# Optimization experiments

Measured on AMD Instinct MI355X. Metric: run time of the kernel, lower is better.

## Reference

```python
import jax, jax.numpy as jnp
import numpy as np

B, L, D, H = 2, 2048, 2048, 16
HD = D // H          # head_dim = 128
LAT = HD // 4        # latent_dim = 32


def setup_inputs() -> dict:
    key = jax.random.key(0)
    ks = jax.random.split(key, 16)
    def w(k, shape, fan_in):
        return jax.random.normal(k, shape, jnp.float32) / np.float32(np.sqrt(fan_in))
    x = jax.random.normal(ks[0], (B, L, D), jnp.float32)
    # RoPE frequencies, stored as (cos, sin) pairs: [L, HD//2, 2]
    inv_freq = 1.0 / (10000.0 ** (np.arange(0, HD, 2, dtype=np.float32) / HD))
    ang = np.outer(np.arange(L, dtype=np.float32), inv_freq)
    freqs_cis = jnp.stack([jnp.asarray(np.cos(ang)), jnp.asarray(np.sin(ang))], axis=-1)
    return dict(
        x=x, freqs_cis=freqs_cis,
        Wq=w(ks[1], (D, D), D), bq=jnp.zeros((D,), jnp.float32),
        Wk=w(ks[2], (D, D), D), bk=jnp.zeros((D,), jnp.float32),
        Wv=w(ks[3], (D, D), D), bv=jnp.zeros((D,), jnp.float32),
        Wqc=w(ks[4], (LAT, HD), HD), bqc=jnp.zeros((LAT,), jnp.float32),
        Wkc=w(ks[5], (LAT, HD), HD), bkc=jnp.zeros((LAT,), jnp.float32),
        Wvc=w(ks[6], (LAT, HD), HD), bvc=jnp.zeros((LAT,), jnp.float32),
        Wd=w(ks[7], (HD, LAT), LAT), bd=jnp.zeros((HD,), jnp.float32),
        Wo=w(ks[8], (D, D), D), bo=jnp.zeros((D,), jnp.float32),
    )


def _rope(t, freqs_cis):
    # t: [B,H,L,HD]; freqs_cis: [L, HD//2, 2] (cos, sin)
    tp = t.reshape(t.shape[:-1] + (HD // 2, 2))
    a, b = tp[..., 0], tp[..., 1]
    cr = freqs_cis[:, :, 0]  # [L, HD//2]
    ci = freqs_cis[:, :, 1]
    ra = a * cr - b * ci
    rb = a * ci + b * cr
    return jnp.stack([ra, rb], axis=-1).reshape(t.shape)


def reference(x, freqs_cis, Wq, bq, Wk, bk, Wv, bv, Wqc, bqc, Wkc, bkc, Wvc, bvc, Wd, bd, Wo, bo):
    Bx, Lx, Dx = x.shape
    # QKV projections -> [B,H,L,HD]
    def proj(W, bias):
        return (x @ W.T + bias).reshape(Bx, Lx, H, HD).transpose(0, 2, 1, 3)
    q = proj(Wq, bq)
    k = proj(Wk, bk)
    v = proj(Wv, bv)
    q = _rope(q, freqs_cis)
    k = _rope(k, freqs_cis)
    # per-head compression to latent dim: [B,H,L,LAT]
    qc = q @ Wqc.T + bqc
    kc = k @ Wkc.T + bkc
    vc = v @ Wvc.T + bvc
    scores = jnp.einsum('bhie,bhje->bhij', qc, kc) / np.float32(np.sqrt(LAT))
    mask = jnp.triu(jnp.ones((Lx, Lx), bool), 1)  # future positions
    scores = jnp.where(mask, jnp.float32(-jnp.inf), scores)
    probs = jax.nn.softmax(scores, axis=-1)
    attn = jnp.einsum('bhij,bhje->bhie', probs, vc)  # [B,H,L,LAT]
    attn = attn @ Wd.T + bd                          # decompress -> [B,H,L,HD]
    attn = attn.transpose(0, 2, 1, 3).reshape(Bx, Lx, Dx)
    return attn @ Wo.T + bo
```

## Files before the change

kernel.cpp:

```cpp
#include <hip/hip_runtime.h>

typedef __attribute__((ext_vector_type(8))) __bf16 bf16x8;
typedef __attribute__((ext_vector_type(4))) __bf16 bf16x4;
typedef __attribute__((ext_vector_type(4))) float f32x4;
typedef __attribute__((ext_vector_type(16))) float f32x16;

#define LL 2048
#define DD 2048
#define HH 16
#define HDIM 128

__global__ __launch_bounds__(256)
void cvt_all(const float* __restrict__ x, const float* __restrict__ Wq,
             const float* __restrict__ Wk, const float* __restrict__ Wqc,
             const float* __restrict__ Wkc,
             __bf16* __restrict__ xb, __bf16* __restrict__ Wqb, __bf16* __restrict__ Wkb,
             __bf16* __restrict__ Wqcb, __bf16* __restrict__ Wkcb)
{
    size_t i = (size_t)blockIdx.x * 256 + threadIdx.x;
    const float* s; __bf16* d; size_t off;
    if (i < 2097152)      { s = x;   d = xb;   off = i; }
    else if (i < 3145728) { s = Wq;  d = Wqb;  off = i - 2097152; }
    else if (i < 4194304) { s = Wk;  d = Wkb;  off = i - 3145728; }
    else if (i < 4195328) { s = Wqc; d = Wqcb; off = i - 4194304; }
    else                  { s = Wkc; d = Wkcb; off = i - 4195328; }
    float4 v = *(const float4*)(s + off * 4);
    bf16x4 o = { (__bf16)v.x, (__bf16)v.y, (__bf16)v.z, (__bf16)v.w };
    *(bf16x4*)(d + off * 4) = o;
}

__global__ __launch_bounds__(256)
void build_wv_eff(const float* __restrict__ Wv, const float* __restrict__ Wvc,
                  const float* __restrict__ bv, const float* __restrict__ bvc,
                  __bf16* __restrict__ Wveff, float* __restrict__ bveff)
{
    __shared__ float WvcT[128][32];
    const int h = blockIdx.x, dc = blockIdx.y, tid = threadIdx.x;
    for (int i = tid; i < 4096; i += 256) WvcT[i & 127][i >> 7] = Wvc[i];
    __syncthreads();
    const int d  = dc * 64 + (tid & 63);
    const int o0 = (tid >> 6) * 8;
    float acc[8] = {};
    for (int j = 0; j < 128; ++j) {
        const float w = Wv[(size_t)(h * 128 + j) * 2048 + d];
        #pragma unroll
        for (int o = 0; o < 8; ++o) acc[o] += WvcT[j][o0 + o] * w;
    }
    #pragma unroll
    for (int o = 0; o < 8; ++o)
        Wveff[(size_t)(h * 32 + o0 + o) * 2048 + d] = (__bf16)acc[o];
    if (dc == 0 && tid < 32) {
        float s = bvc[tid];
        for (int j = 0; j < 128; ++j) s += WvcT[j][tid] * bv[h * 128 + j];
        bveff[h * 32 + tid] = s;
    }
}

__global__ __launch_bounds__(256)
void build_wo_eff(const float* __restrict__ Wo, const float* __restrict__ Wd,
                  __bf16* __restrict__ Woeff)
{
    __shared__ float WdL[128][32];
    const int dc = blockIdx.x, h = blockIdx.y, tid = threadIdx.x;
    for (int i = tid; i < 4096; i += 256) WdL[i >> 5][i & 31] = Wd[i];
    __syncthreads();
    const int dout = dc * 64 + (tid & 63);
    const int o0   = (tid >> 6) * 8;
    float acc[8] = {};
    const float* wrow = Wo + (size_t)dout * 2048 + h * 128;
    for (int u = 0; u < 128; ++u) {
        const float w = wrow[u];
        #pragma unroll
        for (int o = 0; o < 8; ++o) acc[o] += WdL[u][o0 + o] * w;
    }
    #pragma unroll
    for (int o = 0; o < 8; ++o)
        Woeff[(size_t)dout * 512 + h * 32 + o0 + o] = (__bf16)acc[o];
}

__global__ __launch_bounds__(256)
void build_bo_eff(const float* __restrict__ Wo, const float* __restrict__ bd,
                  const float* __restrict__ bo, float* __restrict__ boeff)
{
    __shared__ float bdL[128];
    const int tid = threadIdx.x;
    if (tid < 128) bdL[tid] = bd[tid];
    __syncthreads();
    const int d  = blockIdx.x * 32 + (tid >> 3);
    const int s0 = (tid & 7) * 64;
    float s = 0.f;
    const float* wrow = Wo + (size_t)d * 2048 + s0 * 4;
    for (int c4 = 0; c4 < 64; ++c4) {
        float4 wv = *(const float4*)(wrow + c4 * 4);
        const int cb = ((s0 + c4) * 4) & 127;
        s += wv.x * bdL[cb] + wv.y * bdL[cb + 1] + wv.z * bdL[cb + 2] + wv.w * bdL[cb + 3];
    }
    #pragma unroll
    for (int off = 4; off; off >>= 1) s += __shfl_down(s, off, 8);
    if ((tid & 7) == 0) boeff[d] = bo[d] + s;
}

typedef unsigned int u32;
typedef const __attribute__((address_space(1))) u32* gp_t;
typedef __attribute__((address_space(3))) u32* lp_t;
__device__ __forceinline__ void gload16(const __bf16* g, __bf16* l)
{
    __builtin_amdgcn_global_load_lds((gp_t)(const void*)g, (lp_t)(void*)l, 16, 0, 0);
}

#define MF16(a, b, c) __builtin_amdgcn_mfma_f32_16x16x32_bf16(a, b, c, 0, 0, 0)

__global__ __launch_bounds__(512, 2)
void gemm_qkv8(const __bf16* __restrict__ A,
               const __bf16* __restrict__ Wq, const __bf16* __restrict__ Wk,
               const __bf16* __restrict__ Wveff,
               const float* __restrict__ bq, const float* __restrict__ bk,
               const float* __restrict__ bveff,
               __bf16* __restrict__ qb, __bf16* __restrict__ kb, __bf16* __restrict__ vt)
{
    __shared__ __bf16 lds[4][2][8192];

    const int bid = blockIdx.x;
    const int xcd = bid & 7;
    const int jj  = bid >> 3;
    const int by  = xcd * 2 + (jj / 18);
    const int bx  = jj % 18;
    const int m0  = by * 256;
    const int which = (bx >= 16) ? 2 : (bx >> 3);
    const int nseg  = (which == 2) ? (bx - 16) * 256 : (bx & 7) * 256;
    const __bf16* W = which == 0 ? Wq : which == 1 ? Wk : Wveff;

    const int tid  = threadIdx.x;
    const int wid  = tid >> 6;
    const int lane = tid & 63;
    const int wr   = wid >> 2;
    const int wc   = wid & 3;
    const int l15  = lane & 15;
    const int l4   = lane >> 4;
    const int swz  = (l4 ^ (l15 & 3)) * 8;

    const int srl  = lane >> 2;
    const int scol = ((lane & 3) ^ (srl & 3)) * 8;
    const __bf16* gA0 = A + (size_t)(m0 + wid * 32 + srl) * 2048 + scol;
    const __bf16* gA1 = gA0 + (size_t)16 * 2048;
    const __bf16* gB0 = W + (size_t)(nseg + wid * 32 + srl) * 2048 + scol;
    const __bf16* gB1 = gB0 + (size_t)16 * 2048;

    #define STAGE_A(bb, kkv)                                           \
    {   __bf16* d_ = &lds[bb][0][(wid * 2) * 512];                     \
        gload16(gA0 + (kkv), d_);                                      \
        gload16(gA1 + (kkv), d_ + 512);                                \
    }
    #define STAGE_B(bb, kkv)                                           \
    {   __bf16* d_ = &lds[bb][1][(wid * 2) * 512];                     \
        gload16(gB0 + (kkv), d_);                                      \
        gload16(gB1 + (kkv), d_ + 512);                                \
    }
    #define RD_A(bb, mf) (*(const bf16x8*)&lds[bb][0][(wr * 128 + (mf) * 16 + l15) * 32 + swz])
    #define RD_B(bb, nf) (*(const bf16x8*)&lds[bb][1][(wc * 64 + (nf) * 16 + l15) * 32 + swz])

    f32x4 acc[8][4] = {};

    STAGE_A(0, 0)  STAGE_B(0, 0)
    STAGE_A(1, 32) STAGE_B(1, 32)
    STAGE_A(2, 64) STAGE_B(2, 64)

    #define TILE_BODY(bb, VMS, DOSTAGE, kkv)                                  \
    {                                                                         \
        const int b_ = (bb);                                                  \
        asm volatile("s_waitcnt vmcnt(" VMS ")" ::: "memory");                \
        __builtin_amdgcn_s_barrier();                                         \
        bf16x8 fa[8], fb[4];                                                  \
        _Pragma("unroll")                                                     \
        for (int mf = 0; mf < 8; ++mf) fa[mf] = RD_A(b_, mf);                 \
        fb[0] = RD_B(b_, 0); fb[1] = RD_B(b_, 1);                             \
        if (DOSTAGE) STAGE_A(((b_ + 3) & 3), (kkv))                           \
        asm volatile("s_waitcnt lgkmcnt(0)" ::: "memory");                    \
        __builtin_amdgcn_sched_barrier(0);                                    \
        __builtin_amdgcn_s_setprio(1);                                        \
        _Pragma("unroll")                                                     \
        for (int mf = 0; mf < 8; ++mf) {                                      \
            acc[mf][0] = MF16(fa[mf], fb[0], acc[mf][0]);                     \
            acc[mf][1] = MF16(fa[mf], fb[1], acc[mf][1]);                     \
        }                                                                     \
        __builtin_amdgcn_s_setprio(0);                                        \
        fb[2] = RD_B(b_, 2); fb[3] = RD_B(b_, 3);                             \
        if (DOSTAGE) STAGE_B(((b_ + 3) & 3), (kkv))                           \
        asm volatile("s_waitcnt lgkmcnt(0)" ::: "memory");                    \
        __builtin_amdgcn_sched_barrier(0);                                    \
        __builtin_amdgcn_s_setprio(1);                                        \
        _Pragma("unroll")                                                     \
        for (int mf = 0; mf < 8; ++mf) {                                      \
            acc[mf][2] = MF16(fa[mf], fb[2], acc[mf][2]);                     \
            acc[mf][3] = MF16(fa[mf], fb[3], acc[mf][3]);                     \
        }                                                                     \
        __builtin_amdgcn_s_setprio(0);                                        \
    }

    for (int t = 0; t < 61; ++t)
        TILE_BODY((t & 3), "8", true, (t + 3) * 32)
    TILE_BODY(1, "8", false, 0)
    TILE_BODY(2, "4", false, 0)
    TILE_BODY(3, "0", false, 0)

    #undef TILE_BODY
    #undef STAGE_A
    #undef STAGE_B
    #undef RD_A
    #undef RD_B

    if (which < 2) {
        __bf16* C = which ? kb : qb;
        const float* bb = which ? bk : bq;
        #pragma unroll
        for (int nf = 0; nf < 4; ++nf) {
            const int col = nseg + wc * 64 + nf * 16 + l15;
            const float bv = bb[col];
            #pragma unroll
            for (int mf = 0; mf < 8; ++mf) {
                const int row0 = m0 + wr * 128 + mf * 16 + l4 * 4;
                #pragma unroll
                for (int rr = 0; rr < 4; ++rr)
                    C[(size_t)(row0 + rr) * 2048 + col] = (__bf16)(acc[mf][nf][rr] + bv);
            }
        }
    } else {
        #pragma unroll
        for (int nf = 0; nf < 4; ++nf) {
            const int ncol = nseg + wc * 64 + nf * 16 + l15;
            const float bv = bveff[ncol];
            const int hh = ncol >> 5, oo = ncol & 31;
            #pragma unroll
            for (int mf = 0; mf < 8; ++mf) {
                const int row0 = m0 + wr * 128 + mf * 16 + l4 * 4;
                const int b = row0 >> 11, l0 = row0 & 2047;
                bf16x4 pk = { (__bf16)(acc[mf][nf][0] + bv), (__bf16)(acc[mf][nf][1] + bv),
                              (__bf16)(acc[mf][nf][2] + bv), (__bf16)(acc[mf][nf][3] + bv) };
                *(bf16x4*)(vt + ((size_t)((b * 16 + hh) * 32 + oo)) * 2048 + l0) = pk;
            }
        }
    }
}

__global__ __launch_bounds__(256)
void gemm_ao(const __bf16* __restrict__ ao, const __bf16* __restrict__ Woeff,
             const float* __restrict__ boeff, float* __restrict__ out)
{
    __shared__ __bf16 As[128][64];
    __shared__ __bf16 Bs[128][64];
    const int bid = blockIdx.x;
    const int x   = bid & 7;
    const int jj  = bid >> 3;
    const int bx  = x * 2 + (jj & 1);
    const int by  = jj >> 1;
    const int m0  = by * 128;
    const int n0  = bx * 128;

    const int tid  = threadIdx.x;
    const int wave = tid >> 6;
    const int lane = tid & 63;
    const int wr   = (wave >> 1) * 64;
    const int wc   = (wave & 1) * 64;
    const int lr   = lane & 15;
    const int lk   = (lane >> 4) * 8;
    const int srow = wave * 32 + (lane >> 3);
    const int scol = (lane & 7) * 8;

    f32x4 acc[4][4] = {};
    __bf16* lA = &As[wave * 32][0];
    __bf16* lB = &Bs[wave * 32][0];
    const __bf16* Ww = Woeff + (size_t)(n0 + srow) * 512 + scol;

    for (int k0 = 0; k0 < 512; k0 += 64) {
        const int kk = k0 + scol;
        const int hblk = kk >> 5, oo = kk & 31;
        #pragma unroll
        for (int j = 0; j < 4; ++j) {
            const int r = m0 + srow + j * 8;
            const int b = r >> 11, l = r & 2047;
            gload16(ao + ((size_t)((b << 4) + hblk) * 2048 + l) * 32 + oo, lA + j * 512);
            gload16(Ww + (size_t)(j * 8) * 512 + k0, lB + j * 512);
        }
        __syncthreads();
        #pragma unroll
        for (int ks = 0; ks < 2; ++ks) {
            bf16x8 af[4], bfr[4];
            #pragma unroll
            for (int m = 0; m < 4; ++m)
                af[m] = *(const bf16x8*)(&As[wr + m * 16 + lr][ks * 32 + lk]);
            #pragma unroll
            for (int n = 0; n < 4; ++n)
                bfr[n] = *(const bf16x8*)(&Bs[wc + n * 16 + lr][ks * 32 + lk]);
            #pragma unroll
            for (int m = 0; m < 4; ++m)
                #pragma unroll
                for (int n = 0; n < 4; ++n)
                    acc[m][n] = MF16(af[m], bfr[n], acc[m][n]);
        }
        __syncthreads();
    }

    const int orow = (lane >> 4) * 4;
    #pragma unroll
    for (int n = 0; n < 4; ++n) {
        const int col = n0 + wc + n * 16 + lr;
        const float bv = boeff[col];
        #pragma unroll
        for (int m = 0; m < 4; ++m) {
            #pragma unroll
            for (int r = 0; r < 4; ++r) {
                const int row = m0 + wr + m * 16 + orow + r;
                out[(size_t)row * 2048 + col] = acc[m][n][r] + bv;
            }
        }
    }
}

__global__ __launch_bounds__(256)
void latproj_mfma(const __bf16* __restrict__ qb, const __bf16* __restrict__ kb,
                  const __bf16* __restrict__ Wqcb, const __bf16* __restrict__ Wkcb,
                  const float* __restrict__ bq, const float* __restrict__ bk,
                  const float* __restrict__ fc,
                  __bf16* __restrict__ qc, __bf16* __restrict__ kc)
{
    const int which = blockIdx.y;
    const __bf16* in = which == 0 ? qb : kb;
    const __bf16* Wb = which == 0 ? Wqcb : Wkcb;
    const float*  bs = which == 0 ? bq : bk;

    const int wave = threadIdx.x >> 6;
    const int lane = threadIdx.x & 63;
    const int o    = lane & 31;
    const int hi   = lane >> 5;
    const int g0   = (blockIdx.x * 4 + wave) * 32;

    bf16x8 wf[8];
    #pragma unroll
    for (int ks = 0; ks < 8; ++ks)
        wf[ks] = *(const bf16x8*)(Wb + o * 128 + ks * 16 + hi * 8);

    const int g = g0 + o;
    const int b = g >> 15, h = (g >> 11) & 15, l = g & (LL - 1);
    const __bf16* arow = in + ((size_t)(b * LL + l)) * DD + h * HDIM;
    const float* fcr = fc + (size_t)l * 128;

    f32x16 C = {};
    #pragma unroll
    for (int ks = 0; ks < 8; ++ks) {
        bf16x8 af = *(const bf16x8*)(arow + ks * 16 + hi * 8);
        const float4 cA = *(const float4*)(fcr + (ks * 8 + hi * 4) * 2);
        const float4 cB = *(const float4*)(fcr + (ks * 8 + hi * 4) * 2 + 4);
        float a, bb_;
        a = (float)af[0]; bb_ = (float)af[1];
        af[0] = (__bf16)(a * cA.x - bb_ * cA.y); af[1] = (__bf16)(a * cA.y + bb_ * cA.x);
        a = (float)af[2]; bb_ = (float)af[3];
        af[2] = (__bf16)(a * cA.z - bb_ * cA.w); af[3] = (__bf16)(a * cA.w + bb_ * cA.z);
        a = (float)af[4]; bb_ = (float)af[5];
        af[4] = (__bf16)(a * cB.x - bb_ * cB.y); af[5] = (__bf16)(a * cB.y + bb_ * cB.x);
        a = (float)af[6]; bb_ = (float)af[7];
        af[6] = (__bf16)(a * cB.z - bb_ * cB.w); af[7] = (__bf16)(a * cB.w + bb_ * cB.z);
        C = __builtin_amdgcn_mfma_f32_32x32x16_bf16(af, wf[ks], C, 0, 0, 0);
    }

    const float bias = bs[o];
    const float QSCALE = 0.17677669529663689f * 1.44269504088896340f;
    __bf16* outp = (which == 0 ? qc : kc);
    #pragma unroll
    for (int r = 0; r < 16; ++r) {
        const int ro = (r & 3) + 8 * (r >> 2) + 4 * hi;
        float v = C[r] + bias;
        if (which == 0) v *= QSCALE;
        outp[(size_t)(g0 + ro) * 32 + o] = (__bf16)v;
    }
}

__device__ __forceinline__ unsigned pkbf2(float a, float b)
{
    union { __bf16 h[2]; unsigned u; } x;
    x.h[0] = (__bf16)a; x.h[1] = (__bf16)b;
    return x.u;
}

#if __has_builtin(__builtin_amdgcn_permlane32_swap)
typedef unsigned int uint2v __attribute__((ext_vector_type(2)));
__device__ __forceinline__ void plswap(unsigned a, unsigned b, unsigned& w_lo, unsigned& w_hi, int)
{
    uint2v r = __builtin_amdgcn_permlane32_swap(a, b, false, false);
    w_lo = r[0]; w_hi = r[1];
}
#else
__device__ __forceinline__ void plswap(unsigned a, unsigned b, unsigned& w_lo, unsigned& w_hi, int hi)
{
    unsigned ax = (unsigned)__shfl_xor((int)a, 32);
    unsigned bx = (unsigned)__shfl_xor((int)b, 32);
    w_lo = hi ? bx : a;
    w_hi = hi ? b  : ax;
}
#endif

__global__ __launch_bounds__(64)
void attn_part(const __bf16* __restrict__ qc, const __bf16* __restrict__ kc,
               const __bf16* __restrict__ vt,
               float* __restrict__ pm, float* __restrict__ pl, float* __restrict__ po)
{
    const int id  = blockIdx.x;
    const int bhl = id & 7;
    const int c   = id >> 3;
    const int bhh = c / 160;
    const int lin = c - bhh * 160;
    int s, ci;
    if (lin < 16)      { s = lin; ci = 0; }
    else if (lin < 48) { int q = lin - 16; s = 16 + (q >> 1); ci = q & 1; }
    else if (lin < 96) { int q = lin - 48; int d = q / 3; s = 32 + d; ci = q - d * 3; }
    else               { int q = lin - 96; s = 48 + (q >> 2); ci = q & 3; }
    const int bh = bhh * 8 + bhl;

    const int lane = threadIdx.x;
    const int qcol = lane & 31;
    const int hi   = lane >> 5;

    const __bf16* qbase = qc + ((size_t)bh * LL + (size_t)s * 32) * 32;
    const __bf16* kbase = kc + (size_t)bh * LL * 32;
    const __bf16* vbase = vt + (size_t)bh * 32 * LL;

    const bf16x8 qf0 = *(const bf16x8*)(qbase + qcol * 32 + hi * 8);
    const bf16x8 qf1 = *(const bf16x8*)(qbase + qcol * 32 + 16 + hi * 8);

    float m = -1e30f, lsum = 0.f;
    f32x16 O = {};

    const int t0 = ci * 16;
    const int t1 = min(s, t0 + 15);

    const __bf16* krow = kbase + (size_t)(t0 * 32 + qcol) * 32 + hi * 8;
    const __bf16* vrow = vbase + (size_t)qcol * LL + t0 * 32 + hi * 8;
    bf16x8 kc0 = *(const bf16x8*)(krow);
    bf16x8 kc1 = *(const bf16x8*)(krow + 16);
    bf16x8 vc0 = *(const bf16x8*)(vrow);
    bf16x8 vc1 = *(const bf16x8*)(vrow + 16);

    for (int t = t0; t <= t1; ++t) {
        const int tn = (t < t1) ? t + 1 : t;
        const __bf16* krn = kbase + (size_t)(tn * 32 + qcol) * 32 + hi * 8;
        const __bf16* vrn = vbase + (size_t)qcol * LL + tn * 32 + hi * 8;
        bf16x8 kn0 = *(const bf16x8*)(krn);
        bf16x8 kn1 = *(const bf16x8*)(krn + 16);
        bf16x8 vn0 = *(const bf16x8*)(vrn);
        bf16x8 vn1 = *(const bf16x8*)(vrn + 16);

        f32x16 S = {};
        S = __builtin_amdgcn_mfma_f32_32x32x16_bf16(kc0, qf0, S, 0, 0, 0);
        S = __builtin_amdgcn_mfma_f32_32x32x16_bf16(kc1, qf1, S, 0, 0, 0);

        if (t == s) {
            #pragma unroll
            for (int r = 0; r < 16; ++r) {
                const int kl = (r & 3) + 8 * (r >> 2) + 4 * hi;
                if (kl > qcol) S[r] = -1e30f;
            }
        }
        float tm = S[0];
        #pragma unroll
        for (int r = 1; r < 16; ++r) tm = fmaxf(tm, S[r]);
        tm = fmaxf(tm, __shfl_xor(tm, 32));
        const float mn = fmaxf(m, tm);
        const float fr = exp2f(m - mn);
        m = mn;
        float p[16]; float ls = 0.f;
        #pragma unroll
        for (int r = 0; r < 16; ++r) { p[r] = exp2f(S[r] - m); ls += p[r]; }
        lsum = lsum * fr + ls;
        #pragma unroll
        for (int r = 0; r < 16; ++r) O[r] *= fr;

        unsigned w[8];
        #pragma unroll
        for (int i = 0; i < 8; ++i) w[i] = pkbf2(p[2 * i], p[2 * i + 1]);
        union PF { unsigned u[4]; bf16x8 v; } pf1, pf2;
        plswap(w[0], w[2], pf1.u[0], pf1.u[2], hi);
        plswap(w[1], w[3], pf1.u[1], pf1.u[3], hi);
        plswap(w[4], w[6], pf2.u[0], pf2.u[2], hi);
        plswap(w[5], w[7], pf2.u[1], pf2.u[3], hi);

        O = __builtin_amdgcn_mfma_f32_32x32x16_bf16(vc0, pf1.v, O, 0, 0, 0);
        O = __builtin_amdgcn_mfma_f32_32x32x16_bf16(vc1, pf2.v, O, 0, 0, 0);

        kc0 = kn0; kc1 = kn1; vc0 = vn0; vc1 = vn1;
    }

    const float L = lsum + __shfl_xor(lsum, 32);
    const size_t g = (size_t)bh * LL + (size_t)s * 32 + qcol;
    const size_t slot = g * 4 + ci;
    if (hi == 0) { pm[slot] = m; pl[slot] = L; }
    float* pp = po + slot * 32;
    #pragma unroll
    for (int g4 = 0; g4 < 4; ++g4) {
        float4 v = { O[g4 * 4 + 0], O[g4 * 4 + 1], O[g4 * 4 + 2], O[g4 * 4 + 3] };
        *(float4*)(pp + g4 * 8 + 4 * hi) = v;
    }
}

__global__ __launch_bounds__(256)
void attn_comb(const float* __restrict__ pm, const float* __restrict__ pl,
               const float* __restrict__ po, __bf16* __restrict__ ao)
{
    const int g = blockIdx.x * 256 + threadIdx.x;
    const int i = g & (LL - 1);
    const int nch = (i >> 9) + 1;
    float m = -1e30f;
    for (int c = 0; c < nch; ++c) m = fmaxf(m, pm[(size_t)g * 4 + c]);
    float L = 0.f;
    float o[32] = {};
    for (int c = 0; c < nch; ++c) {
        const float w = exp2f(pm[(size_t)g * 4 + c] - m);
        L += w * pl[(size_t)g * 4 + c];
        const float* pp = po + ((size_t)g * 4 + c) * 32;
        #pragma unroll
        for (int d4 = 0; d4 < 8; ++d4) {
            float4 v = *(const float4*)(pp + d4 * 4);
            o[d4*4+0] += w * v.x; o[d4*4+1] += w * v.y;
            o[d4*4+2] += w * v.z; o[d4*4+3] += w * v.w;
        }
    }
    const float inv = 1.f / L;
    #pragma unroll
    for (int d8 = 0; d8 < 4; ++d8) {
        bf16x8 v;
        #pragma unroll
        for (int j = 0; j < 8; ++j) v[j] = (__bf16)(o[d8 * 8 + j] * inv);
        *(bf16x8*)(ao + (size_t)g * 32 + d8 * 8) = v;
    }
}

extern "C" void kernel_launch(void* const* d_in, const int* in_sizes, int n_in,
                              void* d_out, int out_size, void* d_ws, size_t ws_size,
                              hipStream_t stream)
{
    const float* x   = (const float*)d_in[0];
    const float* fc  = (const float*)d_in[1];
    const float* Wq  = (const float*)d_in[2];
    const float* bq  = (const float*)d_in[3];
    const float* Wk  = (const float*)d_in[4];
    const float* bk  = (const float*)d_in[5];
    const float* Wv  = (const float*)d_in[6];
    const float* bv  = (const float*)d_in[7];
    const float* Wqc = (const float*)d_in[8];
    const float* bqc = (const float*)d_in[9];
    const float* Wkc = (const float*)d_in[10];
    const float* bkc = (const float*)d_in[11];
    const float* Wvc = (const float*)d_in[12];
    const float* bvc = (const float*)d_in[13];
    const float* Wd  = (const float*)d_in[14];
    const float* bd  = (const float*)d_in[15];
    const float* Wo  = (const float*)d_in[16];
    const float* bo  = (const float*)d_in[17];
    float* out = (float*)d_out;

    const size_t MB = 1048576;
    char* w = (char*)d_ws;
    __bf16* xb    = (__bf16*)(w);
    __bf16* Wqb   = (__bf16*)(w + 16 * MB);
    __bf16* Wkb   = (__bf16*)(w + 24 * MB);
    __bf16* Wveff = (__bf16*)(w + 32 * MB);
    __bf16* qb    = (__bf16*)(w + 34 * MB);
    __bf16* kb    = (__bf16*)(w + 50 * MB);
    __bf16* qcbf  = (__bf16*)(w + 66 * MB);
    __bf16* kcbf  = (__bf16*)(w + 70 * MB);
    __bf16* vtbf  = (__bf16*)(w + 74 * MB);
    __bf16* aobf  = (__bf16*)(w + 78 * MB);
    __bf16* Wqcb  = (__bf16*)(w + 82 * MB);
    __bf16* Wkcb  = (__bf16*)(w + 82 * MB + 8192);
    __bf16* Woeff = (__bf16*)(w + 83 * MB);
    float*  boeff = (float*)(w + 85 * MB);
    float*  bveff = (float*)(w + 85 * MB + 8192);

    float* po = (float*)d_ws;
    float* pm = (float*)(w + 32 * MB);
    float* pl = (float*)(w + 33 * MB);

    if (ws_size < (size_t)90 * MB) return;

    cvt_all<<<16392, 256, 0, stream>>>(x, Wq, Wk, Wqc, Wkc, xb, Wqb, Wkb, Wqcb, Wkcb);
    build_wv_eff<<<dim3(16, 32), 256, 0, stream>>>(Wv, Wvc, bv, bvc, Wveff, bveff);
    build_wo_eff<<<dim3(32, 16), 256, 0, stream>>>(Wo, Wd, Woeff);
    build_bo_eff<<<64, 256, 0, stream>>>(Wo, bd, bo, boeff);

    gemm_qkv8<<<288, 512, 0, stream>>>(xb, Wqb, Wkb, Wveff, bq, bk, bveff, qb, kb, vtbf);

    latproj_mfma<<<dim3(512, 2), 256, 0, stream>>>(qb, kb, Wqcb, Wkcb, bqc, bkc, fc,
                                                   qcbf, kcbf);

    attn_part<<<5120, 64, 0, stream>>>(qcbf, kcbf, vtbf, pm, pl, po);
    attn_comb<<<256, 256, 0, stream>>>(pm, pl, po, aobf);

    gemm_ao<<<512, 256, 0, stream>>>(aobf, Woeff, boeff, out);
}
```

Measured before the change: 258.2 us.

## Shrink QKV GEMM tiles to 128x128 with 3-stage pipeline and more blocks

Replaces the 256x256-tile, 512-thread, 4-buffer QKV GEMM with a 128x128-tile, 256-thread kernel using a 3-buffer LDS ring and one barrier per K-step, launched as 1152 blocks instead of 288. The intent is better load balance across CUs, since 288 blocks underfill a 256-CU part in two waves, and higher occupancy (3 blocks per CU). The trade-off is lower arithmetic intensity per tile and more global and L2 traffic for A and W.

```diff
diff --git a/kernel.cpp b/kernel.cpp
--- a/kernel.cpp
+++ b/kernel.cpp
@@ -110,31 +110,32 @@
 
 #define MF16(a, b, c) __builtin_amdgcn_mfma_f32_16x16x32_bf16(a, b, c, 0, 0, 0)
 
-__global__ __launch_bounds__(512, 2)
-void gemm_qkv8(const __bf16* __restrict__ A,
-               const __bf16* __restrict__ Wq, const __bf16* __restrict__ Wk,
-               const __bf16* __restrict__ Wveff,
-               const float* __restrict__ bq, const float* __restrict__ bk,
-               const float* __restrict__ bveff,
-               __bf16* __restrict__ qb, __bf16* __restrict__ kb, __bf16* __restrict__ vt)
-{
-    __shared__ __bf16 lds[4][2][8192];
+__global__ __launch_bounds__(256, 3)
+void gemm_qkv(const __bf16* __restrict__ A,
+              const __bf16* __restrict__ Wq, const __bf16* __restrict__ Wk,
+              const __bf16* __restrict__ Wveff,
+              const float* __restrict__ bq, const float* __restrict__ bk,
+              const float* __restrict__ bveff,
+              __bf16* __restrict__ qb, __bf16* __restrict__ kb, __bf16* __restrict__ vt)
+{
+    __shared__ __bf16 lds[3][2][4096];
 
     const int bid = blockIdx.x;
     const int xcd = bid & 7;
-    const int jj  = bid >> 3;
-    const int by  = xcd * 2 + (jj / 18);
-    const int bx  = jj % 18;
-    const int m0  = by * 256;
-    const int which = (bx >= 16) ? 2 : (bx >> 3);
-    const int nseg  = (which == 2) ? (bx - 16) * 256 : (bx & 7) * 256;
+    const int j   = bid >> 3;
+    const int byl = j / 36;
+    const int bx  = j - byl * 36;
+    const int by  = byl * 8 + xcd;
+    const int m0  = by * 128;
+    const int which = (bx >= 32) ? 2 : (bx >> 4);
+    const int n0  = (which == 2) ? (bx - 32) * 128 : (bx & 15) * 128;
     const __bf16* W = which == 0 ? Wq : which == 1 ? Wk : Wveff;
 
     const int tid  = threadIdx.x;
     const int wid  = tid >> 6;
     const int lane = tid & 63;
-    const int wr   = wid >> 2;
-    const int wc   = wid & 3;
+    const int wr   = wid >> 1;
+    const int wc   = wid & 1;
     const int l15  = lane & 15;
     const int l4   = lane >> 4;
     const int swz  = (l4 ^ (l15 & 3)) * 8;
@@ -142,70 +143,58 @@
     const int srl  = lane >> 2;
     const int scol = ((lane & 3) ^ (srl & 3)) * 8;
     const __bf16* gA0 = A + (size_t)(m0 + wid * 32 + srl) * 2048 + scol;
-    const __bf16* gA1 = gA0 + (size_t)16 * 2048;
-    const __bf16* gB0 = W + (size_t)(nseg + wid * 32 + srl) * 2048 + scol;
-    const __bf16* gB1 = gB0 + (size_t)16 * 2048;
-
-    #define STAGE_A(bb, kkv)                                           \
-    {   __bf16* d_ = &lds[bb][0][(wid * 2) * 512];                     \
-        gload16(gA0 + (kkv), d_);                                      \
-        gload16(gA1 + (kkv), d_ + 512);                                \
-    }
-    #define STAGE_B(bb, kkv)                                           \
-    {   __bf16* d_ = &lds[bb][1][(wid * 2) * 512];                     \
-        gload16(gB0 + (kkv), d_);                                      \
-        gload16(gB1 + (kkv), d_ + 512);                                \
-    }
-    #define RD_A(bb, mf) (*(const bf16x8*)&lds[bb][0][(wr * 128 + (mf) * 16 + l15) * 32 + swz])
+    const __bf16* gB0 = W + (size_t)(n0 + wid * 32 + srl) * 2048 + scol;
+
+    #define STAGE(bb, kk)                                                \
+    {   __bf16* dA = &lds[bb][0][wid * 1024];                            \
+        __bf16* dB = &lds[bb][1][wid * 1024];                            \
+        gload16(gA0 + (kk), dA);                                         \
+        gload16(gA0 + (size_t)16 * 2048 + (kk), dA + 512);               \
+        gload16(gB0 + (kk), dB);                                         \
+        gload16(gB0 + (size_t)16 * 2048 + (kk), dB + 512);               \
+    }
+    #define RD_A(bb, mf) (*(const bf16x8*)&lds[bb][0][(wr * 64 + (mf) * 16 + l15) * 32 + swz])
     #define RD_B(bb, nf) (*(const bf16x8*)&lds[bb][1][(wc * 64 + (nf) * 16 + l15) * 32 + swz])
 
-    f32x4 acc[8][4] = {};
-
-    STAGE_A(0, 0)  STAGE_B(0, 0)
-    STAGE_A(1, 32) STAGE_B(1, 32)
-    STAGE_A(2, 64) STAGE_B(2, 64)
-
-    #define TILE_BODY(bb, VMS, DOSTAGE, kkv)                                  \
+    f32x4 acc[4][4] = {};
+
+    STAGE(0, 0) STAGE(1, 32)
+    asm volatile("s_waitcnt vmcnt(4)" ::: "memory");
+    __builtin_amdgcn_s_barrier();
+
+    #define TB(RB, SB, VM, DOST, kk)                                          \
     {                                                                         \
-        const int b_ = (bb);                                                  \
-        asm volatile("s_waitcnt vmcnt(" VMS ")" ::: "memory");                \
-        __builtin_amdgcn_s_barrier();                                         \
-        bf16x8 fa[8], fb[4];                                                  \
-        _Pragma("unroll")                                                     \
-        for (int mf = 0; mf < 8; ++mf) fa[mf] = RD_A(b_, mf);                 \
-        fb[0] = RD_B(b_, 0); fb[1] = RD_B(b_, 1);                             \
-        if (DOSTAGE) STAGE_A(((b_ + 3) & 3), (kkv))                           \
+        bf16x8 fa[4], fb[4];                                                  \
+        fa[0] = RD_A(RB, 0); fa[1] = RD_A(RB, 1);                             \
+        fa[2] = RD_A(RB, 2); fa[3] = RD_A(RB, 3);                             \
+        fb[0] = RD_B(RB, 0); fb[1] = RD_B(RB, 1);                             \
+        fb[2] = RD_B(RB, 2); fb[3] = RD_B(RB, 3);                             \
+        if (DOST) STAGE(SB, kk)                                               \
         asm volatile("s_waitcnt lgkmcnt(0)" ::: "memory");                    \
         __builtin_amdgcn_sched_barrier(0);                                    \
         __builtin_amdgcn_s_setprio(1);                                        \
         _Pragma("unroll")                                                     \
-        for (int mf = 0; mf < 8; ++mf) {                                      \
-            acc[mf][0] = MF16(fa[mf], fb[0], acc[mf][0]);                     \
-            acc[mf][1] = MF16(fa[mf], fb[1], acc[mf][1]);                     \
-        }                                                                     \
+        for (int mf = 0; mf < 4; ++mf)                                        \
+            _Pragma("unroll")                                                 \
+            for (int nf = 0; nf < 4; ++nf)                                    \
+                acc[mf][nf] = MF16(fa[mf], fb[nf], acc[mf][nf]);              \
         __builtin_amdgcn_s_setprio(0);                                        \
-        fb[2] = RD_B(b_, 2); fb[3] = RD_B(b_, 3);                             \
-        if (DOSTAGE) STAGE_B(((b_ + 3) & 3), (kkv))                           \
-        asm volatile("s_waitcnt lgkmcnt(0)" ::: "memory");                    \
-        __builtin_amdgcn_sched_barrier(0);                                    \
-        __builtin_amdgcn_s_setprio(1);                                        \
-        _Pragma("unroll")                                                     \
-        for (int mf = 0; mf < 8; ++mf) {                                      \
-            acc[mf][2] = MF16(fa[mf], fb[2], acc[mf][2]);                     \
-            acc[mf][3] = MF16(fa[mf], fb[3], acc[mf][3]);                     \
-        }                                                                     \
-        __builtin_amdgcn_s_setprio(0);                                        \
-    }
-
-    for (int t = 0; t < 61; ++t)
-        TILE_BODY((t & 3), "8", true, (t + 3) * 32)
-    TILE_BODY(1, "8", false, 0)
-    TILE_BODY(2, "4", false, 0)
-    TILE_BODY(3, "0", false, 0)
-
-    #undef TILE_BODY
-    #undef STAGE_A
-    #undef STAGE_B
+        asm volatile("s_waitcnt vmcnt(" VM ")" ::: "memory");                 \
+        __builtin_amdgcn_s_barrier();                                         \
+    }
+
+    for (int tt = 0; tt < 60; tt += 3) {
+        const int kk = (tt + 2) * 32;
+        TB(0, 2, "4", true, kk)
+        TB(1, 0, "4", true, kk + 32)
+        TB(2, 1, "4", true, kk + 64)
+    }
+    TB(0, 2, "4", true, 62 * 32)
+    TB(1, 0, "4", true, 63 * 32)
+    TB(2, 0, "0", false, 0)
+    TB(0, 0, "0", false, 0)
+    #undef TB
+    #undef STAGE
     #undef RD_A
     #undef RD_B
 
@@ -214,11 +203,11 @@
         const float* bb = which ? bk : bq;
         #pragma unroll
         for (int nf = 0; nf < 4; ++nf) {
-            const int col = nseg + wc * 64 + nf * 16 + l15;
+            const int col = n0 + wc * 64 + nf * 16 + l15;
             const float bv = bb[col];
             #pragma unroll
-            for (int mf = 0; mf < 8; ++mf) {
-                const int row0 = m0 + wr * 128 + mf * 16 + l4 * 4;
+            for (int mf = 0; mf < 4; ++mf) {
+                const int row0 = m0 + wr * 64 + mf * 16 + l4 * 4;
                 #pragma unroll
                 for (int rr = 0; rr < 4; ++rr)
                     C[(size_t)(row0 + rr) * 2048 + col] = (__bf16)(acc[mf][nf][rr] + bv);
@@ -227,12 +216,12 @@
     } else {
         #pragma unroll
         for (int nf = 0; nf < 4; ++nf) {
-            const int ncol = nseg + wc * 64 + nf * 16 + l15;
+            const int ncol = n0 + wc * 64 + nf * 16 + l15;
             const float bv = bveff[ncol];
             const int hh = ncol >> 5, oo = ncol & 31;
             #pragma unroll
-            for (int mf = 0; mf < 8; ++mf) {
-                const int row0 = m0 + wr * 128 + mf * 16 + l4 * 4;
+            for (int mf = 0; mf < 4; ++mf) {
+                const int row0 = m0 + wr * 64 + mf * 16 + l4 * 4;
                 const int b = row0 >> 11, l0 = row0 & 2047;
                 bf16x4 pk = { (__bf16)(acc[mf][nf][0] + bv), (__bf16)(acc[mf][nf][1] + bv),
                               (__bf16)(acc[mf][nf][2] + bv), (__bf16)(acc[mf][nf][3] + bv) };
@@ -585,7 +574,7 @@
     build_wo_eff<<<dim3(32, 16), 256, 0, stream>>>(Wo, Wd, Woeff);
     build_bo_eff<<<64, 256, 0, stream>>>(Wo, bd, bo, boeff);
 
-    gemm_qkv8<<<288, 512, 0, stream>>>(xb, Wqb, Wkb, Wveff, bq, bk, bveff, qb, kb, vtbf);
+    gemm_qkv<<<1152, 256, 0, stream>>>(xb, Wqb, Wkb, Wveff, bq, bk, bveff, qb, kb, vtbf);
 
     latproj_mfma<<<dim3(512, 2), 256, 0, stream>>>(qb, kb, Wqcb, Wkcb, bqc, bkc, fc,
                                                    qcbf, kcbf);
```

After: 247.4 us. 1.04x faster.
